# Kernel tuning notes

Measured on AMD Instinct MI355X. Metric: run time of the kernel, lower is better.

The kernel has to match this reference:

```python
import jax, jax.numpy as jnp
import numpy as np

H = 64  # lstm_units
FORGET_BIAS = 1.0  # TF LSTMCell default


def setup_inputs() -> dict:
    key = jax.random.key(0)
    k1, k2, k3 = jax.random.split(key, 3)
    B, T = 256, 2048
    x = jax.random.normal(k1, (B, T, 1), dtype=jnp.float32)
    # Layer 1: LSTMCell(64), input dim 1 -> kernel [(1+64), 4*64]
    W1 = jax.random.normal(k2, (1 + H, 4 * H), dtype=jnp.float32) * 0.1
    b1 = jnp.zeros((4 * H,), dtype=jnp.float32)
    # Layer 2: LSTMCell(1), input dim 64 -> kernel [(64+1), 4*1]
    W2 = jax.random.normal(k3, (H + 1, 4), dtype=jnp.float32) * 0.1
    b2 = jnp.zeros((4,), dtype=jnp.float32)
    return {"x": x, "W1": W1, "b1": b1, "W2": W2, "b2": b2}


def _lstm_step(c, h, xt, W, b):
    # TF LSTMCell: gates from concat([x, h]) @ W + b, order i, j, f, o
    z = jnp.concatenate([xt, h], axis=-1) @ W + b
    i, j, f, o = jnp.split(z, 4, axis=-1)
    c_new = jax.nn.sigmoid(f + FORGET_BIAS) * c + jax.nn.sigmoid(i) * jnp.tanh(j)
    h_new = jax.nn.sigmoid(o) * jnpp_tanh(c_new) if False else jax.nn.sigmoid(o) * jnp.tanh(c_new)
    return c_new, h_new


def reference(x, W1, b1, W2, b2):
    # x: [B, T, 1] -> outputs of 2-layer stacked LSTM, final layer size 1
    B = x.shape[0]

    def step(carry, xt):
        c1, h1, c2, h2 = carry
        c1, h1 = _lstm_step(c1, h1, xt, W1, b1)
        c2, h2 = _lstm_step(c2, h2, h1, W2, b2)
        return (c1, h1, c2, h2), h2

    init = (
        jnp.zeros((B, H), x.dtype),
        jnp.zeros((B, H), x.dtype),
        jnp.zeros((B, 1), x.dtype),
        jnp.zeros((B, 1), x.dtype),
    )
    x_tbf = jnp.swapaxes(x, 0, 1)  # [T, B, 1]
    _, ys = jax.lax.scan(step, init, x_tbf)  # ys: [T, B, 1]
    return jnp.swapaxes(ys, 0, 1)  # [B, T, 1]
```

## Files before the change

kernel.cpp:

```cpp
#include <hip/hip_runtime.h>

constexpr int kT = 2048;
constexpr int kB = 256;
constexpr int kH = 64;

__device__ __forceinline__ float fast_sig(float x) {
    return __builtin_amdgcn_rcpf(1.0f + __expf(-x));
}
__device__ __forceinline__ float fast_tanh(float x) {
    float t = __expf(2.0f * x);
    return 1.0f - 2.0f * __builtin_amdgcn_rcpf(t + 1.0f);
}

__global__ __launch_bounds__(320)
__attribute__((amdgpu_waves_per_eu(1)))
void lstm2_kernel(
    const float* __restrict__ x, const float* __restrict__ W1,
    const float* __restrict__ b1, const float* __restrict__ W2,
    const float* __restrict__ b2, float* __restrict__ out)
{
    __shared__ float x_lds[kT];
    __shared__ float h1_lds[2][kH];

    const int tid = threadIdx.x;
    const int b = blockIdx.x;
    const float* xg = x + (size_t)b * kT;
    float* outg = out + (size_t)b * kT;

    for (int i = tid; i < kT; i += 320) x_lds[i] = xg[i];
    if (tid < kH) { h1_lds[0][tid] = 0.0f; h1_lds[1][tid] = 0.0f; }

    const int w = tid >> 6;
    const int l = tid & 63;

    float w0 = 0.0f, b1g = 0.0f;
    float4 wh4[16];
    #pragma unroll
    for (int k = 0; k < 16; ++k) wh4[k] = make_float4(0.f, 0.f, 0.f, 0.f);
    float c1 = 0.0f;
    int u = 0, g = 0;

    float w2p0 = 0, w2p1 = 0, w2p2 = 0, w2p3 = 0;
    float4 w2t = {0, 0, 0, 0}, b2v = {0, 0, 0, 0};
    float c2 = 0.0f, h2 = 0.0f;
    float zi_s = 0, zj_s = 0, zf_s = 0, zo_s = 0;

    if (w < 4) {
        g = l >> 4;
        u = 16 * w + (l & 15);
        const int col = g * 64 + u;
        w0 = W1[col];
        b1g = b1[col];
        #pragma unroll
        for (int k = 0; k < 16; ++k) {
            wh4[k].x = W1[(4 * k + 1) * 256 + col];
            wh4[k].y = W1[(4 * k + 2) * 256 + col];
            wh4[k].z = W1[(4 * k + 3) * 256 + col];
            wh4[k].w = W1[(4 * k + 4) * 256 + col];
        }
    } else {
        const int s = l & 15, gg = l >> 4;
        w2p0 = W2[(s +  0) * 4 + gg];
        w2p1 = W2[(s + 16) * 4 + gg];
        w2p2 = W2[(s + 32) * 4 + gg];
        w2p3 = W2[(s + 48) * 4 + gg];
        w2t = ((const float4*)W2)[kH];
        b2v = ((const float4*)b2)[0];
    }

    #pragma unroll
    for (int k = 0; k < 16; ++k)
        asm volatile("" : "+v"(wh4[k].x), "+v"(wh4[k].y),
                          "+v"(wh4[k].z), "+v"(wh4[k].w));
    asm volatile("" : "+v"(w0), "+v"(b1g));
    asm volatile("" : "+v"(w2p0), "+v"(w2p1), "+v"(w2p2), "+v"(w2p3));
    asm volatile("" : "+v"(w2t.x), "+v"(w2t.y), "+v"(w2t.z), "+v"(w2t.w));
    asm volatile("" : "+v"(b2v.x), "+v"(b2v.y), "+v"(b2v.z), "+v"(b2v.w));

    __syncthreads();

    int cur = 0;
    for (int t = 0; t < kT; ++t) {
        const int nxt = cur ^ 1;
        if (w < 4) {
            const float xt = x_lds[t];
            float z0 = fmaf(xt, w0, b1g), z1 = 0.0f, z2 = 0.0f, z3 = 0.0f;
            const float4* h4 = (const float4*)h1_lds[cur];
            #pragma unroll
            for (int k = 0; k < 16; ++k) {
                float4 h = h4[k];
                z0 = fmaf(h.x, wh4[k].x, z0);
                z1 = fmaf(h.y, wh4[k].y, z1);
                z2 = fmaf(h.z, wh4[k].z, z2);
                z3 = fmaf(h.w, wh4[k].w, z3);
            }
            float z = (z0 + z1) + (z2 + z3);
            float zz = (g == 1) ? 2.0f * z : ((g == 2) ? z + 1.0f : z);
            float sg = fast_sig(zz);
            float a = (g == 1) ? fmaf(2.0f, sg, -1.0f) : sg;
            const int base = l & 15;
            const float ai = __shfl(a, base);
            const float aj = __shfl(a, base + 16);
            const float af = __shfl(a, base + 32);
            const float ao = __shfl(a, base + 48);
            c1 = fmaf(af, c1, ai * aj);
            const float h1n = ao * fast_tanh(c1);
            if (g == 0) h1_lds[nxt][u] = h1n;
        } else {
            if (t >= 2) {
                const float zi = zi_s + h2 * w2t.x;
                const float zj = zj_s + h2 * w2t.y;
                const float zf = zf_s + h2 * w2t.z;
                const float zo = zo_s + h2 * w2t.w;
                c2 = fast_sig(zf + 1.0f) * c2 + fast_sig(zi) * fast_tanh(zj);
                h2 = fast_sig(zo) * fast_tanh(c2);
                if (l == 0) outg[t - 2] = h2;
            }
            if (t >= 1) {
                const int s = l & 15;
                const float* hb = h1_lds[cur];
                float p = hb[s] * w2p0;
                p = fmaf(hb[s + 16], w2p1, p);
                p = fmaf(hb[s + 32], w2p2, p);
                p = fmaf(hb[s + 48], w2p3, p);
                p += __shfl_xor(p, 1);
                p += __shfl_xor(p, 2);
                p += __shfl_xor(p, 4);
                p += __shfl_xor(p, 8);
                zi_s = __shfl(p, s)      + b2v.x;
                zj_s = __shfl(p, s + 16) + b2v.y;
                zf_s = __shfl(p, s + 32) + b2v.z;
                zo_s = __shfl(p, s + 48) + b2v.w;
            }
        }
        __syncthreads();
        cur = nxt;
    }

    if (w == 4) {
        {
            const float zi = zi_s + h2 * w2t.x;
            const float zj = zj_s + h2 * w2t.y;
            const float zf = zf_s + h2 * w2t.z;
            const float zo = zo_s + h2 * w2t.w;
            c2 = fast_sig(zf + 1.0f) * c2 + fast_sig(zi) * fast_tanh(zj);
            h2 = fast_sig(zo) * fast_tanh(c2);
            if (l == 0) outg[kT - 2] = h2;
        }
        {
            const int s = l & 15;
            const float* hb = h1_lds[cur];
            float p = hb[s] * w2p0;
            p = fmaf(hb[s + 16], w2p1, p);
            p = fmaf(hb[s + 32], w2p2, p);
            p = fmaf(hb[s + 48], w2p3, p);
            p += __shfl_xor(p, 1);
            p += __shfl_xor(p, 2);
            p += __shfl_xor(p, 4);
            p += __shfl_xor(p, 8);
            const float zi = __shfl(p, s)      + b2v.x + h2 * w2t.x;
            const float zj = __shfl(p, s + 16) + b2v.y + h2 * w2t.y;
            const float zf = __shfl(p, s + 32) + b2v.z + h2 * w2t.z;
            const float zo = __shfl(p, s + 48) + b2v.w + h2 * w2t.w;
            c2 = fast_sig(zf + 1.0f) * c2 + fast_sig(zi) * fast_tanh(zj);
            h2 = fast_sig(zo) * fast_tanh(c2);
            if (l == 0) outg[kT - 1] = h2;
        }
    }
}

extern "C" void kernel_launch(void* const* d_in, const int* in_sizes, int n_in,
                              void* d_out, int out_size, void* d_ws, size_t ws_size,
                              hipStream_t stream) {
    const float* x  = (const float*)d_in[0];
    const float* W1 = (const float*)d_in[1];
    const float* b1 = (const float*)d_in[2];
    const float* W2 = (const float*)d_in[3];
    const float* b2 = (const float*)d_in[4];
    float* out = (float*)d_out;
    lstm2_kernel<<<kB, 320, 0, stream>>>(x, W1, b1, W2, b2, out);
}
```

Measured before the change: 1.100 ms.

## Broadcast h1 via readlane, stage outputs in LDS, vectorize x loads

Each layer-1 lane now reads one h1 value from LDS and gets the other 63 by readlane broadcasts, replacing the sixteen float4 LDS reads per step. Per-step global stores of the layer-2 output go to an LDS buffer, which is written to global memory with float4 stores after the loop. The initial x load is also vectorized to float4. The change targets LDS read latency and scattered global writes on the serial recurrence critical path. It costs 64 scalar readlane ops per step plus an extra 8KB of LDS.

```diff
diff --git a/kernel.cpp b/kernel.cpp
--- a/kernel.cpp
+++ b/kernel.cpp
@@ -11,6 +11,9 @@
     float t = __expf(2.0f * x);
     return 1.0f - 2.0f * __builtin_amdgcn_rcpf(t + 1.0f);
 }
+__device__ __forceinline__ float bcast(float v, int lane) {
+    return __int_as_float(__builtin_amdgcn_readlane(__float_as_int(v), lane));
+}
 
 __global__ __launch_bounds__(320)
 __attribute__((amdgpu_waves_per_eu(1)))
@@ -19,15 +22,18 @@
     const float* __restrict__ b1, const float* __restrict__ W2,
     const float* __restrict__ b2, float* __restrict__ out)
 {
-    __shared__ float x_lds[kT];
+    __shared__ float4 x4_lds[kT / 4];
+    __shared__ float4 out4_lds[kT / 4];
     __shared__ float h1_lds[2][kH];
+    float* x_lds = (float*)x4_lds;
+    float* out_lds = (float*)out4_lds;
 
     const int tid = threadIdx.x;
     const int b = blockIdx.x;
-    const float* xg = x + (size_t)b * kT;
-    float* outg = out + (size_t)b * kT;
+    const float4* xg4 = (const float4*)(x + (size_t)b * kT);
+    float4* outg4 = (float4*)(out + (size_t)b * kT);
 
-    for (int i = tid; i < kT; i += 320) x_lds[i] = xg[i];
+    for (int i = tid; i < kT / 4; i += 320) x4_lds[i] = xg4[i];
     if (tid < kH) { h1_lds[0][tid] = 0.0f; h1_lds[1][tid] = 0.0f; }
 
     const int w = tid >> 6;
@@ -84,15 +90,14 @@
         const int nxt = cur ^ 1;
         if (w < 4) {
             const float xt = x_lds[t];
+            const float hv = h1_lds[cur][l];
             float z0 = fmaf(xt, w0, b1g), z1 = 0.0f, z2 = 0.0f, z3 = 0.0f;
-            const float4* h4 = (const float4*)h1_lds[cur];
             #pragma unroll
             for (int k = 0; k < 16; ++k) {
-                float4 h = h4[k];
-                z0 = fmaf(h.x, wh4[k].x, z0);
-                z1 = fmaf(h.y, wh4[k].y, z1);
-                z2 = fmaf(h.z, wh4[k].z, z2);
-                z3 = fmaf(h.w, wh4[k].w, z3);
+                z0 = fmaf(bcast(hv, 4 * k + 0), wh4[k].x, z0);
+                z1 = fmaf(bcast(hv, 4 * k + 1), wh4[k].y, z1);
+                z2 = fmaf(bcast(hv, 4 * k + 2), wh4[k].z, z2);
+                z3 = fmaf(bcast(hv, 4 * k + 3), wh4[k].w, z3);
             }
             float z = (z0 + z1) + (z2 + z3);
             float zz = (g == 1) ? 2.0f * z : ((g == 2) ? z + 1.0f : z);
@@ -114,7 +119,7 @@
                 const float zo = zo_s + h2 * w2t.w;
                 c2 = fast_sig(zf + 1.0f) * c2 + fast_sig(zi) * fast_tanh(zj);
                 h2 = fast_sig(zo) * fast_tanh(c2);
-                if (l == 0) outg[t - 2] = h2;
+                if (l == 0) out_lds[t - 2] = h2;
             }
             if (t >= 1) {
                 const int s = l & 15;
@@ -145,7 +150,7 @@
             const float zo = zo_s + h2 * w2t.w;
             c2 = fast_sig(zf + 1.0f) * c2 + fast_sig(zi) * fast_tanh(zj);
             h2 = fast_sig(zo) * fast_tanh(c2);
-            if (l == 0) outg[kT - 2] = h2;
+            if (l == 0) out_lds[kT - 2] = h2;
         }
         {
             const int s = l & 15;
@@ -164,9 +169,12 @@
             const float zo = __shfl(p, s + 48) + b2v.w + h2 * w2t.w;
             c2 = fast_sig(zf + 1.0f) * c2 + fast_sig(zi) * fast_tanh(zj);
             h2 = fast_sig(zo) * fast_tanh(c2);
-            if (l == 0) outg[kT - 1] = h2;
+            if (l == 0) out_lds[kT - 1] = h2;
         }
     }
+
+    __syncthreads();
+    for (int i = tid; i < kT / 4; i += 320) outg4[i] = out4_lds[i];
 }
 
 extern "C" void kernel_launch(void* const* d_in, const int* in_sizes, int n_in,
```

After: 1.174 ms. +6.7%, slower.
